# Performance work log

Hardware: AMD Instinct MI355X
Metric: run time of the kernel (lower is better)

Reference implementation:

```python
import jax, jax.numpy as jnp
import numpy as np

N_QUBITS = 2
DEPTH = 5
N_SAMPLES = 2097152


def _ry_batch(theta):
    # theta: [N] -> per-sample RY matrices [N,2,2] (real, cast to complex)
    c = jnp.cos(theta / 2)
    s = jnp.sin(theta / 2)
    m = jnp.stack([jnp.stack([c, -s], axis=-1),
                   jnp.stack([s, c], axis=-1)], axis=-2)
    return m.astype(jnp.complex64)


def _rx(theta):
    # theta: scalar -> RX matrix [2,2] complex
    c = jnp.cos(theta / 2).astype(jnp.complex64)
    s = jnp.sin(theta / 2).astype(jnp.complex64)
    return jnp.stack([jnp.stack([c, -1j * s]),
                      jnp.stack([-1j * s, c])])


def _quantum_circuit_batched(x, weights):
    # x: [N,2] angles; weights: [DEPTH,2]. Returns <Z_0> per sample, [N].
    n = x.shape[0]
    # state[n, q0, q1], start in |00>
    state = jnp.zeros((n, 2, 2), dtype=jnp.complex64).at[:, 0, 0].set(1.0)
    # AngleEmbedding: RY(x[:,0]) on wire 0, RY(x[:,1]) on wire 1 (per-sample)
    state = jnp.einsum('nab,nbq->naq', _ry_batch(x[:, 0]), state)
    state = jnp.einsum('nab,npb->npa', _ry_batch(x[:, 1]), state)
    # BasicEntanglerLayers: per layer RX on each wire, then one CNOT(0->1)
    # (PennyLane applies a single CNOT for the 2-wire special case)
    for l in range(DEPTH):
        state = jnp.einsum('ab,nbq->naq', _rx(weights[l, 0]), state)
        state = jnp.einsum('ab,npb->npa', _rx(weights[l, 1]), state)
        # CNOT control=q0, target=q1: flip q1 axis where q0 == 1
        state = jnp.stack([state[:, 0, :], state[:, 1, ::-1]], axis=1)
    prob = state.real ** 2 + state.imag ** 2  # [N,2,2]
    # <Z_0> = P(q0=0) - P(q0=1)
    return prob[:, 0, :].sum(-1) - prob[:, 1, :].sum(-1)


def setup_inputs() -> dict:
    key = jax.random.key(0)
    k1, k2, k3, k4 = jax.random.split(key, 4)
    two_pi = 2.0 * np.pi
    x = jax.random.normal(k1, (N_SAMPLES, N_QUBITS), dtype=jnp.float32)
    q_weights = jax.random.uniform(k2, (DEPTH, N_QUBITS), dtype=jnp.float32) * two_pi
    fc_w = jax.random.normal(k3, (1, 1), dtype=jnp.float32)
    fc_b = jax.random.normal(k4, (1,), dtype=jnp.float32)
    return {"x": x, "q_weights": q_weights, "fc_w": fc_w, "fc_b": fc_b}


def reference(x, q_weights, fc_w, fc_b):
    q_out = _quantum_circuit_batched(x, q_weights)  # [N]
    # nn.Linear(1,1) on q_out[:, None] then sigmoid, then squeeze -> [N]
    return jax.nn.sigmoid(q_out * fc_w[0, 0] + fc_b[0])
```

## Files before the change

kernel.cpp:

```cpp
#include <hip/hip_runtime.h>
#include <math.h>

#define DEPTH 5
#define SPT 8

__global__ __launch_bounds__(256) void hqnet_kernel(
    const float* __restrict__ x, const float* __restrict__ qw,
    const float* __restrict__ fcw, const float* __restrict__ fcb,
    float* __restrict__ out, int n_samples)
{
    __shared__ float uRe[4][4], uIm[4][4];
    __shared__ float s_w, s_b;

    if (threadIdx.x < 4) {
        const int j = threadIdx.x;
        float cr[4], ci[4];
        #pragma unroll
        for (int i = 0; i < 4; i++) { cr[i] = (i == j) ? 1.f : 0.f; ci[i] = 0.f; }
        #pragma unroll
        for (int l = 0; l < DEPTH; l++) {
            float c0, s0, c1, s1;
            __sincosf(qw[2 * l + 0] * 0.5f, &s0, &c0);
            __sincosf(qw[2 * l + 1] * 0.5f, &s1, &c1);
            #pragma unroll
            for (int b = 0; b < 2; b++) {
                float ar = cr[b], ai = ci[b], br = cr[b + 2], bi = ci[b + 2];
                cr[b]     = c0 * ar + s0 * bi;  ci[b]     = c0 * ai - s0 * br;
                cr[b + 2] = c0 * br + s0 * ai;  ci[b + 2] = c0 * bi - s0 * ar;
            }
            #pragma unroll
            for (int a = 0; a < 2; a++) {
                int r0 = 2 * a, r1 = 2 * a + 1;
                float ar = cr[r0], ai = ci[r0], br = cr[r1], bi = ci[r1];
                cr[r0] = c1 * ar + s1 * bi;  ci[r0] = c1 * ai - s1 * br;
                cr[r1] = c1 * br + s1 * ai;  ci[r1] = c1 * bi - s1 * ar;
            }
            float tr = cr[2], ti = ci[2];
            cr[2] = cr[3]; ci[2] = ci[3];
            cr[3] = tr;    ci[3] = ti;
        }
        #pragma unroll
        for (int i = 0; i < 4; i++) { uRe[i][j] = cr[i]; uIm[i][j] = ci[i]; }
        if (j == 0) { s_w = fcw[0]; s_b = fcb[0]; }
    }
    __syncthreads();

    float ur[4][4], ui[4][4];
    #pragma unroll
    for (int i = 0; i < 4; i++)
        #pragma unroll
        for (int j = 0; j < 4; j++) { ur[i][j] = uRe[i][j]; ui[i][j] = uIm[i][j]; }
    const float w = s_w, bb = s_b;

    const int t = blockIdx.x * blockDim.x + threadIdx.x;
    const long long base = (long long)t * SPT;
    if (base >= n_samples) return;

    if (base + SPT <= n_samples) {
        const float4* xv = (const float4*)x;
        float xs[2 * SPT];
        #pragma unroll
        for (int q = 0; q < SPT / 2; q++) {
            float4 v = xv[(SPT / 2) * t + q];
            xs[4 * q + 0] = v.x; xs[4 * q + 1] = v.y;
            xs[4 * q + 2] = v.z; xs[4 * q + 3] = v.w;
        }
        float res[SPT];
        #pragma unroll
        for (int k = 0; k < SPT; k++) {
            float s0, c0, s1, c1;
            __sincosf(xs[2 * k + 0] * 0.5f, &s0, &c0);
            __sincosf(xs[2 * k + 1] * 0.5f, &s1, &c1);
            const float p0 = c0 * c1, p1 = c0 * s1, p2 = s0 * c1, p3 = s0 * s1;
            float zp = 0.f, zn = 0.f;
            #pragma unroll
            for (int i = 0; i < 4; i++) {
                float vr = ur[i][0] * p0 + ur[i][1] * p1 + ur[i][2] * p2 + ur[i][3] * p3;
                float vi = ui[i][0] * p0 + ui[i][1] * p1 + ui[i][2] * p2 + ui[i][3] * p3;
                float pr = vr * vr + vi * vi;
                if (i < 2) zp += pr; else zn += pr;
            }
            res[k] = 1.0f / (1.0f + __expf(-(w * zp - w * zn + bb)));
        }
        float4* ov = (float4*)out;
        #pragma unroll
        for (int q = 0; q < SPT / 4; q++)
            ov[(SPT / 4) * t + q] = make_float4(res[4 * q], res[4 * q + 1],
                                                res[4 * q + 2], res[4 * q + 3]);
    } else {
        for (int k = 0; k < SPT && base + k < n_samples; k++) {
            float s0, c0, s1, c1;
            __sincosf(x[2 * (base + k) + 0] * 0.5f, &s0, &c0);
            __sincosf(x[2 * (base + k) + 1] * 0.5f, &s1, &c1);
            const float p0 = c0 * c1, p1 = c0 * s1, p2 = s0 * c1, p3 = s0 * s1;
            float z = 0.f;
            for (int i = 0; i < 4; i++) {
                float vr = ur[i][0] * p0 + ur[i][1] * p1 + ur[i][2] * p2 + ur[i][3] * p3;
                float vi = ui[i][0] * p0 + ui[i][1] * p1 + ui[i][2] * p2 + ui[i][3] * p3;
                float pr = vr * vr + vi * vi;
                z += (i < 2) ? pr : -pr;
            }
            out[base + k] = 1.0f / (1.0f + __expf(-(z * w + bb)));
        }
    }
}

extern "C" void kernel_launch(void* const* d_in, const int* in_sizes, int n_in,
                              void* d_out, int out_size, void* d_ws, size_t ws_size,
                              hipStream_t stream) {
    const float* x   = (const float*)d_in[0];
    const float* qw  = (const float*)d_in[1];
    const float* fcw = (const float*)d_in[2];
    const float* fcb = (const float*)d_in[3];
    float* out = (float*)d_out;

    const int n_samples = in_sizes[0] / 2;
    const int n_threads = (n_samples + SPT - 1) / SPT;
    const int block = 256;
    const int grid = (n_threads + block - 1) / block;
    hqnet_kernel<<<grid, block, 0, stream>>>(x, qw, fcw, fcb, out, n_samples);
}
```

Measured before the change: 72.66 us.

## Fold circuit into trig-basis quadratic form and use wave-strided coalesced loads

Precomputes per block a 9-coefficient bilinear form in (1,cos x0,sin x0)×(1,cos x1,sin x1), derived from the Hermitian observable U^†ZU. The half angles are absorbed by double-angle identities, and the fc weight, bias and log2e are folded in. Each sample then costs two sincos, six FMAs, one exp2 and one rcp, replacing the complex 4x4 matvec. Loads are restructured so each wave reads four float4 groups strided by 64 lanes for coalescing, with float2 stores. This adds two extra block syncs and single-thread setup work, and uses the approximate rcp and exp2 intrinsics.

```diff
diff --git a/kernel.cpp b/kernel.cpp
--- a/kernel.cpp
+++ b/kernel.cpp
@@ -2,7 +2,18 @@
 #include <math.h>
 
 #define DEPTH 5
-#define SPT 8
+
+
+__device__ __forceinline__ float eval_sample(const float B[9], float x0, float x1) {
+    float s0, c0, s1, c1;
+    __sincosf(x0, &s0, &c0);
+    __sincosf(x1, &s1, &c1);
+    float u0 = fmaf(B[2], s1, fmaf(B[1], c1, B[0]));
+    float u1 = fmaf(B[5], s1, fmaf(B[4], c1, B[3]));
+    float u2 = fmaf(B[8], s1, fmaf(B[7], c1, B[6]));
+    float t = fmaf(s0, u2, fmaf(c0, u1, u0));
+    return __builtin_amdgcn_rcpf(1.0f + __builtin_amdgcn_exp2f(t));
+}
 
 __global__ __launch_bounds__(256) void hqnet_kernel(
     const float* __restrict__ x, const float* __restrict__ qw,
@@ -10,7 +21,8 @@
     float* __restrict__ out, int n_samples)
 {
     __shared__ float uRe[4][4], uIm[4][4];
-    __shared__ float s_w, s_b;
+    __shared__ float sA[4][4];
+    __shared__ float sB[9];
 
     if (threadIdx.x < 4) {
         const int j = threadIdx.x;
@@ -41,67 +53,81 @@
         }
         #pragma unroll
         for (int i = 0; i < 4; i++) { uRe[i][j] = cr[i]; uIm[i][j] = ci[i]; }
-        if (j == 0) { s_w = fcw[0]; s_b = fcb[0]; }
     }
     __syncthreads();
 
-    float ur[4][4], ui[4][4];
+    if (threadIdx.x < 16) {
+        const int i = threadIdx.x >> 2, j = threadIdx.x & 3;
+        float a = 0.f;
+        a += uRe[0][i] * uRe[0][j] + uIm[0][i] * uIm[0][j];
+        a += uRe[1][i] * uRe[1][j] + uIm[1][i] * uIm[1][j];
+        a -= uRe[2][i] * uRe[2][j] + uIm[2][i] * uIm[2][j];
+        a -= uRe[3][i] * uRe[3][j] + uIm[3][i] * uIm[3][j];
+        sA[i][j] = a;
+    }
+    __syncthreads();
+
+    if (threadIdx.x == 0) {
+        float h[2][2][3];
+        #pragma unroll
+        for (int a0 = 0; a0 < 2; a0++)
+            #pragma unroll
+            for (int b0 = 0; b0 < 2; b0++) {
+                float m00 = sA[2 * a0 + 0][2 * b0 + 0], m01 = sA[2 * a0 + 0][2 * b0 + 1];
+                float m10 = sA[2 * a0 + 1][2 * b0 + 0], m11 = sA[2 * a0 + 1][2 * b0 + 1];
+                h[a0][b0][0] = 0.5f * (m00 + m11);
+                h[a0][b0][1] = 0.5f * (m00 - m11);
+                h[a0][b0][2] = 0.5f * (m01 + m10);
+            }
+        const float scale = -1.44269504f * fcw[0];
+        #pragma unroll
+        for (int l = 0; l < 3; l++) {
+            sB[0 * 3 + l] = scale * 0.5f * (h[0][0][l] + h[1][1][l]);
+            sB[1 * 3 + l] = scale * 0.5f * (h[0][0][l] - h[1][1][l]);
+            sB[2 * 3 + l] = scale * 0.5f * (h[0][1][l] + h[1][0][l]);
+        }
+        sB[0] += -1.44269504f * fcb[0];
+    }
+    __syncthreads();
+
+    float B[9];
     #pragma unroll
-    for (int i = 0; i < 4; i++)
+    for (int k = 0; k < 9; k++) B[k] = sB[k];
+
+    const int tid  = blockIdx.x * blockDim.x + threadIdx.x;
+    const int wave = tid >> 6;
+    const int lane = threadIdx.x & 63;
+    const int nF4  = n_samples >> 1;
+    const int f0   = wave * 256 + lane;
+    const float4* __restrict__ xv = (const float4*)x;
+    float2* __restrict__ ov = (float2*)out;
+
+    if (f0 + 192 < nF4) {
+        float4 v0 = xv[f0];
+        float4 v1 = xv[f0 + 64];
+        float4 v2 = xv[f0 + 128];
+        float4 v3 = xv[f0 + 192];
+        float2 r0 = make_float2(eval_sample(B, v0.x, v0.y), eval_sample(B, v0.z, v0.w));
+        float2 r1 = make_float2(eval_sample(B, v1.x, v1.y), eval_sample(B, v1.z, v1.w));
+        float2 r2 = make_float2(eval_sample(B, v2.x, v2.y), eval_sample(B, v2.z, v2.w));
+        float2 r3 = make_float2(eval_sample(B, v3.x, v3.y), eval_sample(B, v3.z, v3.w));
+        ov[f0]       = r0;
+        ov[f0 + 64]  = r1;
+        ov[f0 + 128] = r2;
+        ov[f0 + 192] = r3;
+    } else {
         #pragma unroll
-        for (int j = 0; j < 4; j++) { ur[i][j] = uRe[i][j]; ui[i][j] = uIm[i][j]; }
-    const float w = s_w, bb = s_b;
-
-    const int t = blockIdx.x * blockDim.x + threadIdx.x;
-    const long long base = (long long)t * SPT;
-    if (base >= n_samples) return;
-
-    if (base + SPT <= n_samples) {
-        const float4* xv = (const float4*)x;
-        float xs[2 * SPT];
-        #pragma unroll
-        for (int q = 0; q < SPT / 2; q++) {
-            float4 v = xv[(SPT / 2) * t + q];
-            xs[4 * q + 0] = v.x; xs[4 * q + 1] = v.y;
-            xs[4 * q + 2] = v.z; xs[4 * q + 3] = v.w;
+        for (int q = 0; q < 4; q++) {
+            int f = f0 + 64 * q;
+            if (f < nF4) {
+                float4 v = xv[f];
+                ov[f] = make_float2(eval_sample(B, v.x, v.y), eval_sample(B, v.z, v.w));
+            }
         }
-        float res[SPT];
-        #pragma unroll
-        for (int k = 0; k < SPT; k++) {
-            float s0, c0, s1, c1;
-            __sincosf(xs[2 * k + 0] * 0.5f, &s0, &c0);
-            __sincosf(xs[2 * k + 1] * 0.5f, &s1, &c1);
-            const float p0 = c0 * c1, p1 = c0 * s1, p2 = s0 * c1, p3 = s0 * s1;
-            float zp = 0.f, zn = 0.f;
-            #pragma unroll
-            for (int i = 0; i < 4; i++) {
-                float vr = ur[i][0] * p0 + ur[i][1] * p1 + ur[i][2] * p2 + ur[i][3] * p3;
-                float vi = ui[i][0] * p0 + ui[i][1] * p1 + ui[i][2] * p2 + ui[i][3] * p3;
-                float pr = vr * vr + vi * vi;
-                if (i < 2) zp += pr; else zn += pr;
-            }
-            res[k] = 1.0f / (1.0f + __expf(-(w * zp - w * zn + bb)));
-        }
-        float4* ov = (float4*)out;
-        #pragma unroll
-        for (int q = 0; q < SPT / 4; q++)
-            ov[(SPT / 4) * t + q] = make_float4(res[4 * q], res[4 * q + 1],
-                                                res[4 * q + 2], res[4 * q + 3]);
-    } else {
-        for (int k = 0; k < SPT && base + k < n_samples; k++) {
-            float s0, c0, s1, c1;
-            __sincosf(x[2 * (base + k) + 0] * 0.5f, &s0, &c0);
-            __sincosf(x[2 * (base + k) + 1] * 0.5f, &s1, &c1);
-            const float p0 = c0 * c1, p1 = c0 * s1, p2 = s0 * c1, p3 = s0 * s1;
-            float z = 0.f;
-            for (int i = 0; i < 4; i++) {
-                float vr = ur[i][0] * p0 + ur[i][1] * p1 + ur[i][2] * p2 + ur[i][3] * p3;
-                float vi = ui[i][0] * p0 + ui[i][1] * p1 + ui[i][2] * p2 + ui[i][3] * p3;
-                float pr = vr * vr + vi * vi;
-                z += (i < 2) ? pr : -pr;
-            }
-            out[base + k] = 1.0f / (1.0f + __expf(-(z * w + bb)));
-        }
+    }
+    if ((n_samples & 1) && tid == 0) {
+        int last = n_samples - 1;
+        out[last] = eval_sample(B, x[2 * last], x[2 * last + 1]);
     }
 }
 
@@ -115,7 +141,10 @@
     float* out = (float*)d_out;
 
     const int n_samples = in_sizes[0] / 2;
-    const int n_threads = (n_samples + SPT - 1) / SPT;
+    const int nF4 = n_samples >> 1;
+    int nWaves = (nF4 + 255) >> 8;
+    if (nWaves < 1) nWaves = 1;
+    const int n_threads = nWaves * 64;
     const int block = 256;
     const int grid = (n_threads + block - 1) / block;
     hqnet_kernel<<<grid, block, 0, stream>>>(x, qw, fcw, fcb, out, n_samples);
```

Result: no change. 71.85 us (-1.1%).
